# Performance work log

Measured on AMD Instinct MI355X. Metric: run time of the kernel, lower is better.

## Reference

```python
import jax, jax.numpy as jnp
import numpy as np


def setup_inputs() -> dict:
    key = jax.random.key(0)
    k1, k2, k3, k4 = jax.random.split(key, 4)
    B, S, H, E, I = 2, 2048, 1024, 8, 2048
    return {
        "x": jax.random.normal(k1, (B, S, H), jnp.float32),
        "Wg": jax.random.normal(k2, (H, E), jnp.float32) * 0.02,      # router weight
        "W_in": jax.random.normal(k3, (E, H, 2 * I), jnp.float32) * 0.02,  # gated FFN in
        "W_out": jax.random.normal(k4, (E, I, H), jnp.float32) * 0.02,      # FFN out
        "top_k": 2,
    }


def reference(x, Wg, W_in, W_out, top_k):
    B, S, H = x.shape
    E = Wg.shape[1]
    xt = x.reshape(B * S, H)                      # [T, H]
    T = xt.shape[0]

    # Router: logits -> top-k -> softmax over selected experts -> dense gates
    logits = xt @ Wg                              # [T, E]
    tk_logits, tk_idx = jax.lax.top_k(logits, top_k)
    tk_gates = jax.nn.softmax(tk_logits, axis=1).astype(x.dtype)
    dense_gates = jnp.zeros((T, E), x.dtype).at[jnp.arange(T)[:, None], tk_idx].set(tk_gates)

    # All-experts MLP (calibrate_all_experts path: same math as sparse routing)
    h = jnp.einsum('th,ehd->etd', xt, W_in)       # [E, T, 2I]
    g, u = jnp.split(h, 2, axis=-1)               # gated FFN chunks
    a = jax.nn.silu(g) * u                        # [E, T, I]
    y = jnp.einsum('eti,eih->eth', a, W_out)      # [E, T, H]

    out = jnp.einsum('eth,te->th', y, dense_gates)  # combine with gates
    return out.reshape(B, S, H)
```

## Files before the change

### kernel.cpp

```cpp
#include <hip/hip_runtime.h>
#include <hip/hip_bf16.h>

#define T_TOKENS 4096
#define H_DIM    1024
#define E_EXP    8
#define I_DIM    2048

typedef short bf16x8 __attribute__((ext_vector_type(8)));
typedef float f32x4  __attribute__((ext_vector_type(4)));

#define SWZ(r) (((r) >> 1) & 3)

__device__ inline unsigned short f2bf(float f) {
  union { __hip_bfloat16 h; unsigned short u; } c;
  c.h = __float2bfloat16(f);
  return c.u;
}
__device__ inline float bf2f(unsigned short u) {
  union { unsigned int i; float f; } c;
  c.i = (unsigned int)u << 16;
  return c.f;
}

__device__ inline void load16_lds(const void* g, void* l) {
  __builtin_amdgcn_global_load_lds(
      (const __attribute__((address_space(1))) unsigned int*)g,
      (__attribute__((address_space(3))) unsigned int*)l, 16, 0, 0);
}

__global__ void cast_bf16_kernel(const float* __restrict__ in,
                                 unsigned short* __restrict__ out, int n) {
  int i = (blockIdx.x * blockDim.x + threadIdx.x) * 4;
  if (i >= n) return;
  float4 v = *(const float4*)(in + i);
  ushort4 o;
  o.x = f2bf(v.x); o.y = f2bf(v.y); o.z = f2bf(v.z); o.w = f2bf(v.w);
  *(ushort4*)(out + i) = o;
}

__global__ void cast_transpose_kernel(const float* __restrict__ in,
                                      unsigned short* __restrict__ out,
                                      int K, int N) {
  __shared__ float tile[64][33];
  const float* src = in + (size_t)blockIdx.z * K * N;
  unsigned short* dst = out + (size_t)blockIdx.z * K * N;
  int n0 = blockIdx.x * 32, k0 = blockIdx.y * 64;
  int tid = threadIdx.x;
#pragma unroll
  for (int r = 0; r < 8; r++) {
    int idx = r * 256 + tid;
    int kk = idx >> 5, nn = idx & 31;
    tile[kk][nn] = src[(size_t)(k0 + kk) * N + n0 + nn];
  }
  __syncthreads();
  int n = tid >> 3, kg = tid & 7;
  __align__(16) unsigned short o[8];
#pragma unroll
  for (int j = 0; j < 8; j++) o[j] = f2bf(tile[kg * 8 + j][n]);
  *(uint4*)&dst[(size_t)(n0 + n) * K + k0 + kg * 8] = *(uint4*)o;
}

__global__ void router_kernel(const float* __restrict__ x, const float* __restrict__ Wg,
                              int* __restrict__ counts, int* __restrict__ list_tok,
                              float* __restrict__ list_gate, int* __restrict__ tok_codes) {
  int t = blockIdx.x;
  int lane = threadIdx.x;
  float acc[8];
#pragma unroll
  for (int e = 0; e < 8; e++) acc[e] = 0.f;
  const float* xr = x + (size_t)t * H_DIM;
  for (int h = lane; h < H_DIM; h += 64) {
    float xv = xr[h];
    const float4* w = (const float4*)(Wg + (size_t)h * 8);
    float4 w0 = w[0], w1 = w[1];
    acc[0] += xv * w0.x; acc[1] += xv * w0.y; acc[2] += xv * w0.z; acc[3] += xv * w0.w;
    acc[4] += xv * w1.x; acc[5] += xv * w1.y; acc[6] += xv * w1.z; acc[7] += xv * w1.w;
  }
#pragma unroll
  for (int off = 32; off > 0; off >>= 1)
#pragma unroll
    for (int e = 0; e < 8; e++) acc[e] += __shfl_xor(acc[e], off, 64);
  if (lane == 0) {
    int e1 = 0; float l1 = acc[0];
    for (int e = 1; e < 8; e++) if (acc[e] > l1) { l1 = acc[e]; e1 = e; }
    int e2 = -1; float l2 = -1e30f;
    for (int e = 0; e < 8; e++) if (e != e1 && acc[e] > l2) { l2 = acc[e]; e2 = e; }
    float g1 = 1.f / (1.f + expf(l2 - l1));
    float g2 = 1.f - g1;
    int p1 = atomicAdd(&counts[e1], 1);
    list_tok[e1 * T_TOKENS + p1] = t; list_gate[e1 * T_TOKENS + p1] = g1;
    int p2 = atomicAdd(&counts[e2], 1);
    list_tok[e2 * T_TOKENS + p2] = t; list_gate[e2 * T_TOKENS + p2] = g2;
    tok_codes[2 * t]     = e1 * T_TOKENS + p1;
    tok_codes[2 * t + 1] = e2 * T_TOKENS + p2;
  }
}

__global__ void prefix_kernel(const int* __restrict__ counts, int* __restrict__ base) {
  if (threadIdx.x == 0) {
    int s = 0;
    for (int e = 0; e < 8; e++) { base[e] = s; s += counts[e]; }
  }
}

__global__ __launch_bounds__(256) void gemm1_kernel(
    const unsigned short* __restrict__ xb,
    const unsigned short* __restrict__ w_in_t,
    const int* __restrict__ counts, const int* __restrict__ base,
    const int* __restrict__ list_tok,
    unsigned short* __restrict__ a_buf)
{
  int e = blockIdx.z;
  int Ne = counts[e];
  int row0 = blockIdx.y * 128;
  if (row0 >= Ne) return;
  int ib = blockIdx.x * 64;
  const unsigned short* W = w_in_t + (size_t)e * 4096 * 1024;
  int slot_base = base[e];

  __shared__ __align__(16) unsigned short As[128 * 32];
  __shared__ __align__(16) unsigned short Bs[128 * 32];
  __shared__ int toks[128];

  int tid = threadIdx.x;
  if (tid < 128) {
    int pos = row0 + tid;
    toks[tid] = list_tok[e * T_TOKENS + (pos < Ne ? pos : 0)];
  }
  __syncthreads();

  int wv = tid >> 6, lane = tid & 63;

  const unsigned short* srcA[2];
  const unsigned short* srcB[2];
  unsigned short* ldsA[2];
  unsigned short* ldsB[2];
#pragma unroll
  for (int d = 0; d < 2; d++) {
    int r = 32 * wv + 16 * d + (lane >> 2);
    int kg = (lane & 3) ^ SWZ(r);
    srcA[d] = xb + (size_t)toks[r] * H_DIM + kg * 8;
    int c = r >> 6, q = (r >> 4) & 3, rr = r & 15;
    int wrow = (q & 1) * 2048 + ib + 32 * c + (q >> 1) * 16 + rr;
    srcB[d] = W + (size_t)wrow * H_DIM + kg * 8;
    ldsA[d] = As + (32 * wv + 16 * d) * 32;
    ldsB[d] = Bs + (32 * wv + 16 * d) * 32;
  }

  int rh = wv >> 1, ch = wv & 1;
  int l15 = lane & 15, quad = lane >> 4;

  f32x4 acc[4][4] = {};

  for (int k0 = 0; k0 < H_DIM; k0 += 32) {
    load16_lds(srcA[0] + k0, ldsA[0]);
    load16_lds(srcA[1] + k0, ldsA[1]);
    load16_lds(srcB[0] + k0, ldsB[0]);
    load16_lds(srcB[1] + k0, ldsB[1]);
    __syncthreads();

    bf16x8 af[4], bf[4];
#pragma unroll
    for (int rb = 0; rb < 4; rb++) {
      int row = rh * 64 + rb * 16 + l15;
      int kg = quad ^ SWZ(row);
      af[rb] = *(const bf16x8*)&As[row * 32 + kg * 8];
    }
#pragma unroll
    for (int cb = 0; cb < 4; cb++) {
      int brow = ch * 64 + cb * 16 + l15;
      int kg = quad ^ SWZ(brow);
      bf[cb] = *(const bf16x8*)&Bs[brow * 32 + kg * 8];
    }
#pragma unroll
    for (int rb = 0; rb < 4; rb++)
#pragma unroll
      for (int cb = 0; cb < 4; cb++)
        acc[rb][cb] = __builtin_amdgcn_mfma_f32_16x16x32_bf16(af[rb], bf[cb], acc[rb][cb], 0, 0, 0);
    __syncthreads();
  }

#pragma unroll
  for (int rb = 0; rb < 4; rb++)
#pragma unroll
    for (int cp = 0; cp < 2; cp++) {
      int icol = ib + 32 * ch + cp * 16 + l15;
#pragma unroll
      for (int v = 0; v < 4; v++) {
        int row = rh * 64 + rb * 16 + quad * 4 + v;
        int pos = row0 + row;
        if (pos < Ne) {
          float g = acc[rb][2 * cp][v], u = acc[rb][2 * cp + 1][v];
          float a = g / (1.f + __expf(-g)) * u;
          a_buf[(size_t)(slot_base + pos) * I_DIM + icol] = f2bf(a);
        }
      }
    }
}

__global__ __launch_bounds__(256) void gemm2_kernel(
    const unsigned short* __restrict__ a_buf,
    const unsigned short* __restrict__ w_out_t,
    const int* __restrict__ counts, const int* __restrict__ base,
    const float* __restrict__ list_gate,
    unsigned short* __restrict__ y_buf)
{
  int e = blockIdx.z;
  int Ne = counts[e];
  int row0 = blockIdx.y * 128;
  if (row0 >= Ne) return;
  int hb = blockIdx.x * 128;
  const unsigned short* W = w_out_t + (size_t)e * 1024 * 2048;
  int slot_base = base[e];

  __shared__ __align__(16) unsigned short As[128 * 32];
  __shared__ __align__(16) unsigned short Bs[128 * 32];
  __shared__ float gts[128];

  int tid = threadIdx.x;
  if (tid < 128) {
    int pos = row0 + tid;
    gts[tid] = list_gate[e * T_TOKENS + (pos < Ne ? pos : Ne - 1)];
  }

  int wv = tid >> 6, lane = tid & 63;
  const unsigned short* srcA[2];
  const unsigned short* srcB[2];
  unsigned short* ldsA[2];
  unsigned short* ldsB[2];
#pragma unroll
  for (int d = 0; d < 2; d++) {
    int r = 32 * wv + 16 * d + (lane >> 2);
    int kg = (lane & 3) ^ SWZ(r);
    int pos = row0 + r;
    int slot = slot_base + (pos < Ne ? pos : Ne - 1);
    srcA[d] = a_buf + (size_t)slot * I_DIM + kg * 8;
    srcB[d] = W + (size_t)(hb + r) * I_DIM + kg * 8;
    ldsA[d] = As + (32 * wv + 16 * d) * 32;
    ldsB[d] = Bs + (32 * wv + 16 * d) * 32;
  }

  int rh = wv >> 1, ch = wv & 1;
  int l15 = lane & 15, quad = lane >> 4;

  f32x4 acc[4][4] = {};

  for (int k0 = 0; k0 < I_DIM; k0 += 32) {
    load16_lds(srcA[0] + k0, ldsA[0]);
    load16_lds(srcA[1] + k0, ldsA[1]);
    load16_lds(srcB[0] + k0, ldsB[0]);
    load16_lds(srcB[1] + k0, ldsB[1]);
    __syncthreads();

    bf16x8 af[4], bf[4];
#pragma unroll
    for (int rb = 0; rb < 4; rb++) {
      int row = rh * 64 + rb * 16 + l15;
      int kg = quad ^ SWZ(row);
      af[rb] = *(const bf16x8*)&As[row * 32 + kg * 8];
    }
#pragma unroll
    for (int cb = 0; cb < 4; cb++) {
      int brow = ch * 64 + cb * 16 + l15;
      int kg = quad ^ SWZ(brow);
      bf[cb] = *(const bf16x8*)&Bs[brow * 32 + kg * 8];
    }
#pragma unroll
    for (int rb = 0; rb < 4; rb++)
#pragma unroll
      for (int cb = 0; cb < 4; cb++)
        acc[rb][cb] = __builtin_amdgcn_mfma_f32_16x16x32_bf16(af[rb], bf[cb], acc[rb][cb], 0, 0, 0);
    __syncthreads();
  }

#pragma unroll
  for (int rb = 0; rb < 4; rb++)
#pragma unroll
    for (int cb = 0; cb < 4; cb++) {
      int col = hb + ch * 64 + cb * 16 + l15;
#pragma unroll
      for (int v = 0; v < 4; v++) {
        int row = rh * 64 + rb * 16 + quad * 4 + v;
        int pos = row0 + row;
        if (pos < Ne)
          y_buf[(size_t)(slot_base + pos) * H_DIM + col] = f2bf(gts[row] * acc[rb][cb][v]);
      }
    }
}

__global__ void combine_kernel(const unsigned short* __restrict__ y_buf,
                               const int* __restrict__ tok_codes,
                               const int* __restrict__ base,
                               float* __restrict__ out) {
  int t = blockIdx.x;
  int c0 = tok_codes[2 * t], c1 = tok_codes[2 * t + 1];
  int s0 = base[c0 / T_TOKENS] + (c0 % T_TOKENS);
  int s1 = base[c1 / T_TOKENS] + (c1 % T_TOKENS);
  int h = threadIdx.x * 4;
  ushort4 a = *(const ushort4*)&y_buf[(size_t)s0 * H_DIM + h];
  ushort4 b = *(const ushort4*)&y_buf[(size_t)s1 * H_DIM + h];
  float4 o;
  o.x = bf2f(a.x) + bf2f(b.x);
  o.y = bf2f(a.y) + bf2f(b.y);
  o.z = bf2f(a.z) + bf2f(b.z);
  o.w = bf2f(a.w) + bf2f(b.w);
  *(float4*)&out[(size_t)t * H_DIM + h] = o;
}

extern "C" void kernel_launch(void* const* d_in, const int* in_sizes, int n_in,
                              void* d_out, int out_size, void* d_ws, size_t ws_size,
                              hipStream_t stream) {
  const float* x     = (const float*)d_in[0];
  const float* Wg    = (const float*)d_in[1];
  const float* W_in  = (const float*)d_in[2];
  const float* W_out = (const float*)d_in[3];

  char* ws = (char*)d_ws;
  size_t off = 0;
  auto alloc = [&](size_t bytes) {
    char* p = ws + off;
    off += (bytes + 255) & ~(size_t)255;
    return p;
  };
  unsigned short* xb      = (unsigned short*)alloc((size_t)T_TOKENS * H_DIM * 2);
  unsigned short* w_in_t  = (unsigned short*)alloc((size_t)E_EXP * 2 * I_DIM * H_DIM * 2);
  unsigned short* w_out_t = (unsigned short*)alloc((size_t)E_EXP * H_DIM * I_DIM * 2);
  unsigned short* a_buf   = (unsigned short*)alloc((size_t)2 * T_TOKENS * I_DIM * 2);
  int*   counts    = (int*)alloc(E_EXP * 4);
  int*   base      = (int*)alloc(E_EXP * 4);
  int*   list_tok  = (int*)alloc((size_t)E_EXP * T_TOKENS * 4);
  float* list_gate = (float*)alloc((size_t)E_EXP * T_TOKENS * 4);
  int*   tok_codes = (int*)alloc((size_t)2 * T_TOKENS * 4);
  if (off > ws_size) return;

  unsigned short* y_buf = w_in_t;

  hipMemsetAsync(counts, 0, E_EXP * 4, stream);

  cast_bf16_kernel<<<(T_TOKENS * H_DIM / 4 + 255) / 256, 256, 0, stream>>>(x, xb, T_TOKENS * H_DIM);
  cast_transpose_kernel<<<dim3(4096 / 32, 1024 / 64, E_EXP), 256, 0, stream>>>(W_in, w_in_t, 1024, 4096);
  cast_transpose_kernel<<<dim3(1024 / 32, 2048 / 64, E_EXP), 256, 0, stream>>>(W_out, w_out_t, 2048, 1024);
  router_kernel<<<T_TOKENS, 64, 0, stream>>>(x, Wg, counts, list_tok, list_gate, tok_codes);
  prefix_kernel<<<1, 1, 0, stream>>>(counts, base);
  gemm1_kernel<<<dim3(I_DIM / 64, T_TOKENS / 128, E_EXP), 256, 0, stream>>>(
      xb, w_in_t, counts, base, list_tok, a_buf);
  gemm2_kernel<<<dim3(H_DIM / 128, T_TOKENS / 128, E_EXP), 256, 0, stream>>>(
      a_buf, w_out_t, counts, base, list_gate, y_buf);
  combine_kernel<<<T_TOKENS, 256, 0, stream>>>(y_buf, tok_codes, base, (float*)d_out);
}
```

Baseline: 540.8 us.

## Double-buffer GEMM LDS loads, split-K gemm2, fuse x cast into router

Both expert GEMMs now use double-buffered LDS tiles, so the next K-slice's global-to-LDS load is issued before the current slice's MFMAs. This keeps only one barrier per iteration. The grid is reordered so token-row blocks vary fastest, meaning neighbouring blocks share weight tiles. gemm2 is split into two K halves written to separate partial buffers that combine_kernel sums, which raises parallelism at the cost of extra bf16 partial traffic and an extra rounding. The separate x-to-bf16 cast kernel is removed and folded into the router, which already reads x.

```diff
diff --git a/kernel.cpp b/kernel.cpp
--- a/kernel.cpp
+++ b/kernel.cpp
@@ -26,16 +26,6 @@
   __builtin_amdgcn_global_load_lds(
       (const __attribute__((address_space(1))) unsigned int*)g,
       (__attribute__((address_space(3))) unsigned int*)l, 16, 0, 0);
-}
-
-__global__ void cast_bf16_kernel(const float* __restrict__ in,
-                                 unsigned short* __restrict__ out, int n) {
-  int i = (blockIdx.x * blockDim.x + threadIdx.x) * 4;
-  if (i >= n) return;
-  float4 v = *(const float4*)(in + i);
-  ushort4 o;
-  o.x = f2bf(v.x); o.y = f2bf(v.y); o.z = f2bf(v.z); o.w = f2bf(v.w);
-  *(ushort4*)(out + i) = o;
 }
 
 __global__ void cast_transpose_kernel(const float* __restrict__ in,
@@ -61,6 +51,7 @@
 }
 
 __global__ void router_kernel(const float* __restrict__ x, const float* __restrict__ Wg,
+                              unsigned short* __restrict__ xb,
                               int* __restrict__ counts, int* __restrict__ list_tok,
                               float* __restrict__ list_gate, int* __restrict__ tok_codes) {
   int t = blockIdx.x;
@@ -69,8 +60,10 @@
 #pragma unroll
   for (int e = 0; e < 8; e++) acc[e] = 0.f;
   const float* xr = x + (size_t)t * H_DIM;
+  unsigned short* xbr = xb + (size_t)t * H_DIM;
   for (int h = lane; h < H_DIM; h += 64) {
     float xv = xr[h];
+    xbr[h] = f2bf(xv);
     const float4* w = (const float4*)(Wg + (size_t)h * 8);
     float4 w0 = w[0], w1 = w[1];
     acc[0] += xv * w0.x; acc[1] += xv * w0.y; acc[2] += xv * w0.z; acc[3] += xv * w0.w;
@@ -112,14 +105,14 @@
 {
   int e = blockIdx.z;
   int Ne = counts[e];
-  int row0 = blockIdx.y * 128;
+  int row0 = blockIdx.x * 128;
   if (row0 >= Ne) return;
-  int ib = blockIdx.x * 64;
+  int ib = blockIdx.y * 64;
   const unsigned short* W = w_in_t + (size_t)e * 4096 * 1024;
   int slot_base = base[e];
 
-  __shared__ __align__(16) unsigned short As[128 * 32];
-  __shared__ __align__(16) unsigned short Bs[128 * 32];
+  __shared__ __align__(16) unsigned short As[2][128 * 32];
+  __shared__ __align__(16) unsigned short Bs[2][128 * 32];
   __shared__ int toks[128];
 
   int tid = threadIdx.x;
@@ -133,8 +126,7 @@
 
   const unsigned short* srcA[2];
   const unsigned short* srcB[2];
-  unsigned short* ldsA[2];
-  unsigned short* ldsB[2];
+  int ldsOff[2];
 #pragma unroll
   for (int d = 0; d < 2; d++) {
     int r = 32 * wv + 16 * d + (lane >> 2);
@@ -143,8 +135,7 @@
     int c = r >> 6, q = (r >> 4) & 3, rr = r & 15;
     int wrow = (q & 1) * 2048 + ib + 32 * c + (q >> 1) * 16 + rr;
     srcB[d] = W + (size_t)wrow * H_DIM + kg * 8;
-    ldsA[d] = As + (32 * wv + 16 * d) * 32;
-    ldsB[d] = Bs + (32 * wv + 16 * d) * 32;
+    ldsOff[d] = (32 * wv + 16 * d) * 32;
   }
 
   int rh = wv >> 1, ch = wv & 1;
@@ -152,25 +143,33 @@
 
   f32x4 acc[4][4] = {};
 
+  load16_lds(srcA[0], &As[0][ldsOff[0]]);
+  load16_lds(srcA[1], &As[0][ldsOff[1]]);
+  load16_lds(srcB[0], &Bs[0][ldsOff[0]]);
+  load16_lds(srcB[1], &Bs[0][ldsOff[1]]);
+  __syncthreads();
+
+  int p = 0;
   for (int k0 = 0; k0 < H_DIM; k0 += 32) {
-    load16_lds(srcA[0] + k0, ldsA[0]);
-    load16_lds(srcA[1] + k0, ldsA[1]);
-    load16_lds(srcB[0] + k0, ldsB[0]);
-    load16_lds(srcB[1] + k0, ldsB[1]);
-    __syncthreads();
-
+    int kn = k0 + 32;
+    if (kn < H_DIM) {
+      load16_lds(srcA[0] + kn, &As[1 - p][ldsOff[0]]);
+      load16_lds(srcA[1] + kn, &As[1 - p][ldsOff[1]]);
+      load16_lds(srcB[0] + kn, &Bs[1 - p][ldsOff[0]]);
+      load16_lds(srcB[1] + kn, &Bs[1 - p][ldsOff[1]]);
+    }
     bf16x8 af[4], bf[4];
 #pragma unroll
     for (int rb = 0; rb < 4; rb++) {
       int row = rh * 64 + rb * 16 + l15;
       int kg = quad ^ SWZ(row);
-      af[rb] = *(const bf16x8*)&As[row * 32 + kg * 8];
+      af[rb] = *(const bf16x8*)&As[p][row * 32 + kg * 8];
     }
 #pragma unroll
     for (int cb = 0; cb < 4; cb++) {
       int brow = ch * 64 + cb * 16 + l15;
       int kg = quad ^ SWZ(brow);
-      bf[cb] = *(const bf16x8*)&Bs[brow * 32 + kg * 8];
+      bf[cb] = *(const bf16x8*)&Bs[p][brow * 32 + kg * 8];
     }
 #pragma unroll
     for (int rb = 0; rb < 4; rb++)
@@ -178,6 +177,7 @@
       for (int cb = 0; cb < 4; cb++)
         acc[rb][cb] = __builtin_amdgcn_mfma_f32_16x16x32_bf16(af[rb], bf[cb], acc[rb][cb], 0, 0, 0);
     __syncthreads();
+    p ^= 1;
   }
 
 #pragma unroll
@@ -203,18 +203,20 @@
     const unsigned short* __restrict__ w_out_t,
     const int* __restrict__ counts, const int* __restrict__ base,
     const float* __restrict__ list_gate,
-    unsigned short* __restrict__ y_buf)
+    unsigned short* __restrict__ y_part)
 {
-  int e = blockIdx.z;
+  int e = blockIdx.z >> 1, kh = blockIdx.z & 1;
   int Ne = counts[e];
-  int row0 = blockIdx.y * 128;
+  int row0 = blockIdx.x * 128;
   if (row0 >= Ne) return;
-  int hb = blockIdx.x * 128;
+  int hb = blockIdx.y * 128;
   const unsigned short* W = w_out_t + (size_t)e * 1024 * 2048;
   int slot_base = base[e];
-
-  __shared__ __align__(16) unsigned short As[128 * 32];
-  __shared__ __align__(16) unsigned short Bs[128 * 32];
+  int kbase = kh * 1024;
+  unsigned short* yb = y_part + (size_t)kh * 8192 * 1024;
+
+  __shared__ __align__(16) unsigned short As[2][128 * 32];
+  __shared__ __align__(16) unsigned short Bs[2][128 * 32];
   __shared__ float gts[128];
 
   int tid = threadIdx.x;
@@ -226,18 +228,16 @@
   int wv = tid >> 6, lane = tid & 63;
   const unsigned short* srcA[2];
   const unsigned short* srcB[2];
-  unsigned short* ldsA[2];
-  unsigned short* ldsB[2];
+  int ldsOff[2];
 #pragma unroll
   for (int d = 0; d < 2; d++) {
     int r = 32 * wv + 16 * d + (lane >> 2);
     int kg = (lane & 3) ^ SWZ(r);
     int pos = row0 + r;
     int slot = slot_base + (pos < Ne ? pos : Ne - 1);
-    srcA[d] = a_buf + (size_t)slot * I_DIM + kg * 8;
-    srcB[d] = W + (size_t)(hb + r) * I_DIM + kg * 8;
-    ldsA[d] = As + (32 * wv + 16 * d) * 32;
-    ldsB[d] = Bs + (32 * wv + 16 * d) * 32;
+    srcA[d] = a_buf + (size_t)slot * I_DIM + kbase + kg * 8;
+    srcB[d] = W + (size_t)(hb + r) * I_DIM + kbase + kg * 8;
+    ldsOff[d] = (32 * wv + 16 * d) * 32;
   }
 
   int rh = wv >> 1, ch = wv & 1;
@@ -245,25 +245,33 @@
 
   f32x4 acc[4][4] = {};
 
-  for (int k0 = 0; k0 < I_DIM; k0 += 32) {
-    load16_lds(srcA[0] + k0, ldsA[0]);
-    load16_lds(srcA[1] + k0, ldsA[1]);
-    load16_lds(srcB[0] + k0, ldsB[0]);
-    load16_lds(srcB[1] + k0, ldsB[1]);
-    __syncthreads();
-
+  load16_lds(srcA[0], &As[0][ldsOff[0]]);
+  load16_lds(srcA[1], &As[0][ldsOff[1]]);
+  load16_lds(srcB[0], &Bs[0][ldsOff[0]]);
+  load16_lds(srcB[1], &Bs[0][ldsOff[1]]);
+  __syncthreads();
+
+  int p = 0;
+  for (int k0 = 0; k0 < 1024; k0 += 32) {
+    int kn = k0 + 32;
+    if (kn < 1024) {
+      load16_lds(srcA[0] + kn, &As[1 - p][ldsOff[0]]);
+      load16_lds(srcA[1] + kn, &As[1 - p][ldsOff[1]]);
+      load16_lds(srcB[0] + kn, &Bs[1 - p][ldsOff[0]]);
+      load16_lds(srcB[1] + kn, &Bs[1 - p][ldsOff[1]]);
+    }
     bf16x8 af[4], bf[4];
 #pragma unroll
     for (int rb = 0; rb < 4; rb++) {
       int row = rh * 64 + rb * 16 + l15;
       int kg = quad ^ SWZ(row);
-      af[rb] = *(const bf16x8*)&As[row * 32 + kg * 8];
+      af[rb] = *(const bf16x8*)&As[p][row * 32 + kg * 8];
     }
 #pragma unroll
     for (int cb = 0; cb < 4; cb++) {
       int brow = ch * 64 + cb * 16 + l15;
       int kg = quad ^ SWZ(brow);
-      bf[cb] = *(const bf16x8*)&Bs[brow * 32 + kg * 8];
+      bf[cb] = *(const bf16x8*)&Bs[p][brow * 32 + kg * 8];
     }
 #pragma unroll
     for (int rb = 0; rb < 4; rb++)
@@ -271,6 +279,7 @@
       for (int cb = 0; cb < 4; cb++)
         acc[rb][cb] = __builtin_amdgcn_mfma_f32_16x16x32_bf16(af[rb], bf[cb], acc[rb][cb], 0, 0, 0);
     __syncthreads();
+    p ^= 1;
   }
 
 #pragma unroll
@@ -283,27 +292,30 @@
         int row = rh * 64 + rb * 16 + quad * 4 + v;
         int pos = row0 + row;
         if (pos < Ne)
-          y_buf[(size_t)(slot_base + pos) * H_DIM + col] = f2bf(gts[row] * acc[rb][cb][v]);
+          yb[(size_t)(slot_base + pos) * H_DIM + col] = f2bf(gts[row] * acc[rb][cb][v]);
       }
     }
 }
 
-__global__ void combine_kernel(const unsigned short* __restrict__ y_buf,
+__global__ void combine_kernel(const unsigned short* __restrict__ y_part,
                                const int* __restrict__ tok_codes,
                                const int* __restrict__ base,
                                float* __restrict__ out) {
   int t = blockIdx.x;
   int c0 = tok_codes[2 * t], c1 = tok_codes[2 * t + 1];
-  int s0 = base[c0 / T_TOKENS] + (c0 % T_TOKENS);
-  int s1 = base[c1 / T_TOKENS] + (c1 % T_TOKENS);
+  size_t s0 = (size_t)(base[c0 / T_TOKENS] + (c0 % T_TOKENS)) * H_DIM;
+  size_t s1 = (size_t)(base[c1 / T_TOKENS] + (c1 % T_TOKENS)) * H_DIM;
+  const size_t HALF = (size_t)8192 * 1024;
   int h = threadIdx.x * 4;
-  ushort4 a = *(const ushort4*)&y_buf[(size_t)s0 * H_DIM + h];
-  ushort4 b = *(const ushort4*)&y_buf[(size_t)s1 * H_DIM + h];
+  ushort4 a0 = *(const ushort4*)&y_part[s0 + h];
+  ushort4 a1 = *(const ushort4*)&y_part[HALF + s0 + h];
+  ushort4 b0 = *(const ushort4*)&y_part[s1 + h];
+  ushort4 b1 = *(const ushort4*)&y_part[HALF + s1 + h];
   float4 o;
-  o.x = bf2f(a.x) + bf2f(b.x);
-  o.y = bf2f(a.y) + bf2f(b.y);
-  o.z = bf2f(a.z) + bf2f(b.z);
-  o.w = bf2f(a.w) + bf2f(b.w);
+  o.x = (bf2f(a0.x) + bf2f(a1.x)) + (bf2f(b0.x) + bf2f(b1.x));
+  o.y = (bf2f(a0.y) + bf2f(a1.y)) + (bf2f(b0.y) + bf2f(b1.y));
+  o.z = (bf2f(a0.z) + bf2f(a1.z)) + (bf2f(b0.z) + bf2f(b1.z));
+  o.w = (bf2f(a0.w) + bf2f(a1.w)) + (bf2f(b0.w) + bf2f(b1.w));
   *(float4*)&out[(size_t)t * H_DIM + h] = o;
 }
 
@@ -333,18 +345,17 @@
   int*   tok_codes = (int*)alloc((size_t)2 * T_TOKENS * 4);
   if (off > ws_size) return;
 
-  unsigned short* y_buf = w_in_t;
+  unsigned short* y_part = w_in_t;
 
   hipMemsetAsync(counts, 0, E_EXP * 4, stream);
 
-  cast_bf16_kernel<<<(T_TOKENS * H_DIM / 4 + 255) / 256, 256, 0, stream>>>(x, xb, T_TOKENS * H_DIM);
   cast_transpose_kernel<<<dim3(4096 / 32, 1024 / 64, E_EXP), 256, 0, stream>>>(W_in, w_in_t, 1024, 4096);
   cast_transpose_kernel<<<dim3(1024 / 32, 2048 / 64, E_EXP), 256, 0, stream>>>(W_out, w_out_t, 2048, 1024);
-  router_kernel<<<T_TOKENS, 64, 0, stream>>>(x, Wg, counts, list_tok, list_gate, tok_codes);
+  router_kernel<<<T_TOKENS, 64, 0, stream>>>(x, Wg, xb, counts, list_tok, list_gate, tok_codes);
   prefix_kernel<<<1, 1, 0, stream>>>(counts, base);
-  gemm1_kernel<<<dim3(I_DIM / 64, T_TOKENS / 128, E_EXP), 256, 0, stream>>>(
+  gemm1_kernel<<<dim3(T_TOKENS / 128, I_DIM / 64, E_EXP), 256, 0, stream>>>(
       xb, w_in_t, counts, base, list_tok, a_buf);
-  gemm2_kernel<<<dim3(H_DIM / 128, T_TOKENS / 128, E_EXP), 256, 0, stream>>>(
-      a_buf, w_out_t, counts, base, list_gate, y_buf);
-  combine_kernel<<<T_TOKENS, 256, 0, stream>>>(y_buf, tok_codes, base, (float*)d_out);
-}
+  gemm2_kernel<<<dim3(T_TOKENS / 128, H_DIM / 128, E_EXP * 2), 256, 0, stream>>>(
+      a_buf, w_out_t, counts, base, list_gate, y_part);
+  combine_kernel<<<T_TOKENS, 256, 0, stream>>>(y_part, tok_codes, base, (float*)d_out);
+}
```

New measurement: 926.8 us. 1.71x slower.
